# Kernel optimization log

Measured on AMD Instinct MI355X. Metric: run time of the kernel, lower is better.

Reference implementation:

```python
import jax, jax.numpy as jnp
import numpy as np

N, E = 100000, 800000
D_IN, D_H, D_EMB = 64, 64, 64
L, S = 2, 4
NOISE_SCALE, MIN_U = 0.1, 1e-6


def _xavier(k, shape):
    lim = float(np.sqrt(6.0 / (shape[0] + shape[1])))
    return jax.random.uniform(k, shape, jnp.float32, -lim, lim)


def setup_inputs():
    key = jax.random.key(0)
    ks = jax.random.split(key, 7)
    x = jax.random.normal(ks[0], (N, D_IN), jnp.float32)
    edge_index = jax.random.randint(ks[1], (2, E), 0, N)
    parent_mask = jax.random.bernoulli(ks[2], 0.7, (E,))
    Wi = _xavier(ks[3], (D_IN, D_H))
    bi = jnp.zeros((D_H,), jnp.float32)
    msg_W = jnp.stack([_xavier(jax.random.fold_in(ks[4], l), (2 * D_H, D_H)) for l in range(L)])
    msg_b = jnp.zeros((L, D_H), jnp.float32)
    upd_W = jnp.stack([_xavier(jax.random.fold_in(ks[5], l), (2 * D_H, D_H)) for l in range(L)])
    upd_b = jnp.zeros((L, D_H), jnp.float32)
    Wf = _xavier(ks[6], (D_H, D_EMB))
    bf = jnp.zeros((D_EMB,), jnp.float32)
    return dict(x=x, edge_index=edge_index, parent_mask=parent_mask, Wi=Wi, bi=bi,
                msg_W=msg_W, msg_b=msg_b, upd_W=upd_W, upd_b=upd_b, Wf=Wf, bf=bf)


def _gnn(x, src, dst, mask_f, cnt_inv, Wi, bi, msg_W, msg_b, upd_W, upd_b, Wf, bf):
    # input_proj -> relu, then L rounds of (gather -> message linear -> masked
    # scatter-mean -> update linear -> relu), then final_proj.
    h = jax.nn.relu(x @ Wi + bi)
    for l in range(L):
        Wm, Wu = msg_W[l], upd_W[l]
        # message = Linear(concat(x_i, x_j)); x_i = h[dst] (target), x_j = h[src] (source)
        msg = h[dst] @ Wm[:D_H] + h[src] @ Wm[D_H:] + msg_b[l]  # [E, D_H]
        agg = jax.ops.segment_sum(msg * mask_f[:, None], dst, num_segments=N) * cnt_inv[:, None]
        # update = Linear(concat(x, aggr_out))
        h = jax.nn.relu(h @ Wu[:D_H] + agg @ Wu[D_H:] + upd_b[l])
    return h @ Wf + bf  # [N, D_EMB]


def reference(x, edge_index, parent_mask, Wi, bi, msg_W, msg_b, upd_W, upd_b, Wf, bf):
    src, dst = edge_index[0], edge_index[1]
    mask_f = parent_mask.astype(x.dtype)
    # scatter-mean over causal-parent edges only (0 for nodes without parents, as in PyG)
    cnt = jax.ops.segment_sum(mask_f, dst, num_segments=N)
    cnt_inv = 1.0 / jnp.maximum(cnt, 1.0)
    params = (Wi, bi, msg_W, msg_b, upd_W, upd_b, Wf, bf)
    causal_z = _gnn(x, src, dst, mask_f, cnt_inv, *params)
    # Monte Carlo uncertainty: S perturbed causal embeddings, trace of sample covariance
    noise = jax.random.normal(jax.random.key(42), (S, N, D_IN), x.dtype) * NOISE_SCALE
    zs = jax.lax.map(lambda n: _gnn(x + n, src, dst, mask_f, cnt_inv, *params), noise)  # [S, N, D_EMB]
    mean = zs.mean(axis=0)
    u = jnp.sum((zs - mean[None]) ** 2, axis=(0, 2)) / (S - 1)
    u = jnp.maximum(u, MIN_U)
    return causal_z, u
```

## Files before the change

kernel.cpp:

```cpp
#include <hip/hip_runtime.h>
#include <stdint.h>

#define NN 100000
#define EE 800000
#define GEMM_BX 1563
#define WSTR 72
#define SLAB ((size_t)NN * 64)
#define EDGE_CAP 2304

typedef unsigned short u16;
typedef __attribute__((ext_vector_type(8))) short bf16x8;
typedef __attribute__((ext_vector_type(4))) float f32x4;

__device__ __forceinline__ uint32_t f2bf(float f) {
  uint32_t u = __float_as_uint(f);
  return (u + 0x7fffu + ((u >> 16) & 1u)) >> 16;
}

__device__ __forceinline__ void tf_round(uint32_t& x0, uint32_t& x1, int r) {
  x0 += x1;
  x1 = (x1 << r) | (x1 >> (32 - r));
  x1 ^= x0;
}

__device__ __forceinline__ void threefry_0_42(uint32_t c0, uint32_t c1,
                                              uint32_t& o0, uint32_t& o1) {
  const uint32_t ks0 = 0u, ks1 = 42u, ks2 = 0x1BD11BDAu ^ 42u;
  uint32_t x0 = c0 + ks0, x1 = c1 + ks1;
  tf_round(x0, x1, 13); tf_round(x0, x1, 15); tf_round(x0, x1, 26); tf_round(x0, x1, 6);
  x0 += ks1; x1 += ks2 + 1u;
  tf_round(x0, x1, 17); tf_round(x0, x1, 29); tf_round(x0, x1, 16); tf_round(x0, x1, 24);
  x0 += ks2; x1 += ks0 + 2u;
  tf_round(x0, x1, 13); tf_round(x0, x1, 15); tf_round(x0, x1, 26); tf_round(x0, x1, 6);
  x0 += ks0; x1 += ks1 + 3u;
  tf_round(x0, x1, 17); tf_round(x0, x1, 29); tf_round(x0, x1, 16); tf_round(x0, x1, 24);
  x0 += ks1; x1 += ks2 + 4u;
  tf_round(x0, x1, 13); tf_round(x0, x1, 15); tf_round(x0, x1, 26); tf_round(x0, x1, 6);
  x0 += ks2; x1 += ks0 + 5u;
  o0 = x0; o1 = x1;
}

__device__ __forceinline__ float noise_val(int s, int n, int d) {
  uint32_t f = (uint32_t)s * 6400000u + (uint32_t)n * 64u + (uint32_t)d;
  uint32_t o0, o1;
  threefry_0_42(0u, f, o0, o1);
  uint32_t bits = o0 ^ o1;
  float v = __uint_as_float((bits >> 9) | 0x3f800000u) - 1.0f;
  const float LO = -0.99999994f;
  float u = v * 2.0f + LO;
  u = fmaxf(u, LO);
  float w = -__logf(fmaf(-u, u, 1.0f));
  float ww = w - 2.5f;
  float p = 2.81022636e-08f;
  p = fmaf(p, ww, 3.43273939e-07f);
  p = fmaf(p, ww, -3.5233877e-06f);
  p = fmaf(p, ww, -4.39150654e-06f);
  p = fmaf(p, ww, 0.00021858087f);
  p = fmaf(p, ww, -0.00125372503f);
  p = fmaf(p, ww, -0.00417768164f);
  p = fmaf(p, ww, 0.246640727f);
  p = fmaf(p, ww, 1.50140941f);
  if (__any(w >= 5.0f)) {
    float ws = sqrtf(w) - 3.0f;
    float p2 = -0.000200214257f;
    p2 = fmaf(p2, ws, 0.000100950558f);
    p2 = fmaf(p2, ws, 0.00134934322f);
    p2 = fmaf(p2, ws, -0.00367342844f);
    p2 = fmaf(p2, ws, 0.00573950773f);
    p2 = fmaf(p2, ws, -0.0076224613f);
    p2 = fmaf(p2, ws, 0.00943887047f);
    p2 = fmaf(p2, ws, 1.00167406f);
    p2 = fmaf(p2, ws, 2.83297682f);
    p = (w < 5.0f) ? p : p2;
  }
  return 0.141421356f * (p * u);
}

__device__ __forceinline__ int mask_at(const void* m, int e, int mode) {
  if (mode == 0) return ((const int*)m)[e] != 0;
  if (mode == 1) return ((const unsigned char*)m)[e] != 0;
  return ((const float*)m)[e] != 0.0f;
}

__global__ void k_detect(const unsigned* mw, int* mode_out) {
  __shared__ int nonbin, nonfloat;
  if (threadIdx.x == 0) { nonbin = 0; nonfloat = 0; }
  __syncthreads();
  int lb = 0, lf = 0;
  for (int i = threadIdx.x; i < 4096; i += 256) {
    unsigned v = mw[i];
    if (v > 1u) lb = 1;
    if (v != 0u && v != 0x3F800000u) lf = 1;
  }
  if (lb) atomicOr(&nonbin, 1);
  if (lf) atomicOr(&nonfloat, 1);
  __syncthreads();
  if (threadIdx.x == 0)
    mode_out[0] = (nonbin == 0) ? 0 : ((nonfloat == 0) ? 2 : 1);
}

__global__ void k_count(const void* mask, const int* dst, int* cnt, const int* mode_p) {
  int e = blockIdx.x * 256 + threadIdx.x;
  if (e >= EE) return;
  if (mask_at(mask, e, *mode_p)) atomicAdd(&cnt[dst[e]], 1);
}

__global__ void k_scan_a(const int* cnt, int* blockSums) {
  __shared__ int sd[256];
  int t = threadIdx.x;
  int base = blockIdx.x * 1024 + t * 4;
  int s = 0;
  #pragma unroll
  for (int j = 0; j < 4; ++j) {
    int i = base + j;
    if (i < NN) s += cnt[i];
  }
  sd[t] = s;
  __syncthreads();
  for (int off = 128; off > 0; off >>= 1) {
    if (t < off) sd[t] += sd[t + off];
    __syncthreads();
  }
  if (t == 0) blockSums[blockIdx.x] = sd[0];
}

__global__ void k_scan_b(int* blockSums, int nb, int* total_out) {
  __shared__ int sd[128];
  int t = threadIdx.x;
  int v = (t < nb) ? blockSums[t] : 0;
  sd[t] = v;
  __syncthreads();
  for (int off = 1; off < 128; off <<= 1) {
    int x = (t >= off) ? sd[t - off] : 0;
    __syncthreads();
    sd[t] += x;
    __syncthreads();
  }
  if (t < nb) blockSums[t] = sd[t] - v;
  if (t == 0) total_out[0] = sd[127];
}

__global__ void k_scan_c(const int* cnt, const int* blockOffs, int* row_ptr,
                         int* cursor, float* cinv) {
  __shared__ int sd[256];
  int t = threadIdx.x;
  int base = blockIdx.x * 1024 + t * 4;
  int v[4], s = 0;
  #pragma unroll
  for (int j = 0; j < 4; ++j) {
    int i = base + j;
    v[j] = (i < NN) ? cnt[i] : 0;
    s += v[j];
  }
  sd[t] = s;
  __syncthreads();
  for (int off = 1; off < 256; off <<= 1) {
    int x = (t >= off) ? sd[t - off] : 0;
    __syncthreads();
    sd[t] += x;
    __syncthreads();
  }
  int excl = sd[t] - s + blockOffs[blockIdx.x];
  #pragma unroll
  for (int j = 0; j < 4; ++j) {
    int i = base + j;
    if (i < NN) {
      row_ptr[i] = excl;
      cursor[i] = excl;
      cinv[i] = 1.0f / fmaxf((float)v[j], 1.0f);
    }
    excl += v[j];
  }
}

__global__ void k_fill(const void* mask, const int* src, const int* dst,
                       int* cursor, int* col, const int* mode_p) {
  int e = blockIdx.x * 256 + threadIdx.x;
  if (e >= EE) return;
  if (mask_at(mask, e, *mode_p)) {
    int p = atomicAdd(&cursor[dst[e]], 1);
    col[p] = src[e];
  }
}

__global__ void k_prep(const float* msg_W, const float* msg_b, const float* upd_W,
                       const float* Wi, const float* Wf,
                       u16* Wu1T, u16* A1T, u16* A2T, float* C1,
                       u16* WiT, u16* WfT) {
  int t = threadIdx.x;
  int blk = blockIdx.x;
  if (blk >= 128) {
    const float* W = (blk == 128) ? Wi : Wf;
    u16* WT = (blk == 128) ? WiT : WfT;
    for (int o = t; o < 4096; o += 256) {
      int k = o >> 6, n = o & 63;
      WT[n * 64 + k] = (u16)f2bf(W[k * 64 + n]);
    }
    int l = blk - 128;
    const float* Wu2 = upd_W + l * 8192 + 4096;
    if (t < 64) {
      float acc = 0.f;
      for (int j = 0; j < 64; ++j) acc = fmaf(msg_b[l * 64 + j], Wu2[j * 64 + t], acc);
      C1[l * 64 + t] = acc;
    }
    return;
  }
  int l = blk >> 6, b = blk & 63;
  const float* WmT = msg_W + l * 8192;
  const float* WmB = WmT + 4096;
  const float* Wu1 = upd_W + l * 8192;
  const float* Wu2 = Wu1 + 4096;
  __shared__ float sd1[256], sd2[256];
  int a = t & 63, part = t >> 6;
  float a1 = 0.f, a2 = 0.f;
  #pragma unroll
  for (int jj = 0; jj < 16; ++jj) {
    int j = part * 16 + jj;
    float w2 = Wu2[j * 64 + b];
    a1 = fmaf(WmT[a * 64 + j], w2, a1);
    a2 = fmaf(WmB[a * 64 + j], w2, a2);
  }
  sd1[part * 64 + a] = a1;
  sd2[part * 64 + a] = a2;
  __syncthreads();
  if (t < 64) {
    float s1 = sd1[t] + sd1[64 + t] + sd1[128 + t] + sd1[192 + t];
    float s2 = sd2[t] + sd2[64 + t] + sd2[128 + t] + sd2[192 + t];
    int o = l * 4096 + b * 64 + t;
    A1T[o] = (u16)f2bf(s1);
    A2T[o] = (u16)f2bf(s2);
    Wu1T[o] = (u16)f2bf(Wu1[t * 64 + b]);
  }
}

__device__ __forceinline__ void mm4(const u16* lW, int m16, int q,
                                    bf16x8 a0, bf16x8 a1, f32x4 (&acc)[4]) {
  #pragma unroll
  for (int nt = 0; nt < 4; ++nt) {
    const u16* wp = lW + (nt * 16 + m16) * WSTR + q * 8;
    bf16x8 b0 = *(const bf16x8*)(wp);
    bf16x8 b1 = *(const bf16x8*)(wp + 32);
    acc[nt] = __builtin_amdgcn_mfma_f32_16x16x32_bf16(a0, b0, acc[nt], 0, 0, 0);
    acc[nt] = __builtin_amdgcn_mfma_f32_16x16x32_bf16(a1, b1, acc[nt], 0, 0, 0);
  }
}

__device__ __forceinline__ void stage_W(const u16* __restrict__ WT, u16* lW) {
  int t = threadIdx.x;
  int r = t >> 2, seg = (t & 3) * 16;
  const uint4* p = (const uint4*)(WT + r * 64 + seg);
  uint4 a = p[0], b = p[1];
  *(uint4*)(lW + r * WSTR + seg) = a;
  *(uint4*)(lW + r * WSTR + seg + 8) = b;
}

__device__ __forceinline__ void stage_H(const u16* __restrict__ Hin, int R0, u16* lT) {
  int t = threadIdx.x;
  int r = t >> 2, seg = (t & 3) * 16;
  int gr = R0 + r;
  uint4 a = {0, 0, 0, 0}, b = {0, 0, 0, 0};
  if (gr < NN) {
    const uint4* p = (const uint4*)(Hin + (size_t)gr * 64 + seg);
    a = p[0]; b = p[1];
  }
  *(uint4*)(lT + r * WSTR + seg) = a;
  *(uint4*)(lT + r * WSTR + seg + 8) = b;
}

__global__ __launch_bounds__(256) void k_input(const float* __restrict__ x,
                                               const u16* __restrict__ WiT,
                                               const float* __restrict__ bi,
                                               u16* __restrict__ HoutB) {
  __shared__ __align__(16) u16 lT[64 * WSTR];
  __shared__ __align__(16) u16 lW[64 * WSTR];
  __shared__ float lB[64];
  int t = threadIdx.x;
  int R0 = blockIdx.x * 64;
  int inst = blockIdx.y;
  u16* Hout = HoutB + (size_t)inst * SLAB;
  {
    int r = t >> 2, seg = (t & 3) * 16;
    int gr = R0 + r;
    float v[16];
    if (gr < NN) {
      const float4* xp = (const float4*)(x + (size_t)gr * 64 + seg);
      #pragma unroll
      for (int qq = 0; qq < 4; ++qq) {
        float4 f = xp[qq];
        v[qq * 4 + 0] = f.x; v[qq * 4 + 1] = f.y;
        v[qq * 4 + 2] = f.z; v[qq * 4 + 3] = f.w;
      }
      if (inst > 0) {
        int s = inst - 1;
        #pragma unroll
        for (int j = 0; j < 16; ++j) v[j] += noise_val(s, gr, seg + j);
      }
    } else {
      #pragma unroll
      for (int j = 0; j < 16; ++j) v[j] = 0.f;
    }
    uint32_t pk[8];
    #pragma unroll
    for (int j = 0; j < 8; ++j)
      pk[j] = f2bf(v[2 * j]) | (f2bf(v[2 * j + 1]) << 16);
    uint4 A = {pk[0], pk[1], pk[2], pk[3]};
    uint4 B = {pk[4], pk[5], pk[6], pk[7]};
    *(uint4*)(lT + r * WSTR + seg) = A;
    *(uint4*)(lT + r * WSTR + seg + 8) = B;
  }
  stage_W(WiT, lW);
  if (t < 64) lB[t] = bi[t];
  __syncthreads();
  int l = t & 63, w = t >> 6;
  int m16 = l & 15, q = l >> 4;
  const u16* aRow = lT + (w * 16 + m16) * WSTR + q * 8;
  bf16x8 fa0 = *(const bf16x8*)(aRow);
  bf16x8 fa1 = *(const bf16x8*)(aRow + 32);
  f32x4 acc[4] = {{0.f, 0.f, 0.f, 0.f}, {0.f, 0.f, 0.f, 0.f},
                  {0.f, 0.f, 0.f, 0.f}, {0.f, 0.f, 0.f, 0.f}};
  mm4(lW, m16, q, fa0, fa1, acc);
  #pragma unroll
  for (int nt = 0; nt < 4; ++nt) {
    int c = nt * 16 + m16;
    #pragma unroll
    for (int r_ = 0; r_ < 4; ++r_) {
      int row = w * 16 + q * 4 + r_;
      int gr = R0 + row;
      if (gr < NN) {
        float vv = fmaxf(acc[nt][r_] + lB[c], 0.f);
        Hout[(size_t)gr * 64 + c] = (u16)f2bf(vv);
      }
    }
  }
}

__global__ __launch_bounds__(256) void k_layer(const u16* __restrict__ HinB,
                                               u16* __restrict__ HoutB,
                                               const int* __restrict__ row_ptr,
                                               const int* __restrict__ col,
                                               const float* __restrict__ cinv,
                                               const u16* __restrict__ Wu1T,
                                               const u16* __restrict__ A1T,
                                               const u16* __restrict__ A2T,
                                               const float* __restrict__ b0,
                                               const float* __restrict__ c1) {
  __shared__ __align__(16) u16 lS0[64 * WSTR];
  __shared__ __align__(16) u16 lS1[64 * WSTR];
  __shared__ __align__(16) u16 lW[64 * WSTR];
  __shared__ float lB[128];
  __shared__ float lG[64];
  __shared__ int   lRP[65];
  int* lEdge = (int*)lW;

  int t = threadIdx.x;
  int R0 = blockIdx.x * 64;
  int instBase = blockIdx.y * 2;
  bool two = (instBase + 1) < 5;
  const u16* Hin0 = HinB + (size_t)instBase * SLAB;
  const u16* Hin1 = Hin0 + (two ? SLAB : 0);
  u16* Hout0 = HoutB + (size_t)instBase * SLAB;
  u16* Hout1 = Hout0 + SLAB;

  if (t < 65) {
    int idx = R0 + t;
    if (idx > NN) idx = NN;
    lRP[t] = row_ptr[idx];
  }
  if (t < 64) {
    lB[t] = b0[t];
    lB[64 + t] = c1[t];
  }
  __syncthreads();

  int e0 = lRP[0];
  int nE = lRP[64] - e0;
  bool inLds = (nE <= EDGE_CAP);
  if (inLds) {
    for (int i = t; i < nE; i += 256) lEdge[i] = col[e0 + i];
  }
  if (t < 64) lG[t] = (lRP[t + 1] > lRP[t]) ? 1.f : 0.f;
  __syncthreads();

  {
    int sub = t >> 3, lane8 = t & 7;
    int f0 = lane8 * 8;
    const u16* hb0 = Hin0 + f0;
    const u16* hb1 = Hin1 + f0;
    #pragma unroll
    for (int bb = 0; bb < 2; ++bb) {
      int r = bb * 32 + sub;
      int n = R0 + r;
      float g[8], h[8];
      #pragma unroll
      for (int j = 0; j < 8; ++j) { g[j] = 0.f; h[j] = 0.f; }
      if (n < NN) {
        int e = lRP[r], end = lRP[r + 1];
        int last = end - 1;
        for (; e < end; e += 4) {
          int idx4[4];
          #pragma unroll
          for (int j = 0; j < 4; ++j) {
            int ee = e + j;
            ee = (ee < last) ? ee : last;
            idx4[j] = inLds ? lEdge[ee - e0] : col[ee];
          }
          uint4 P[4];
          #pragma unroll
          for (int j = 0; j < 4; ++j)
            P[j] = *(const uint4*)(hb0 + ((unsigned)idx4[j] << 6));
          uint4 Q[4];
          if (two) {
            #pragma unroll
            for (int j = 0; j < 4; ++j)
              Q[j] = *(const uint4*)(hb1 + ((unsigned)idx4[j] << 6));
          }
          #pragma unroll
          for (int j = 1; j < 4; ++j) {
            bool ok = (e + j) < end;
            P[j].x = ok ? P[j].x : 0u;
            P[j].y = ok ? P[j].y : 0u;
            P[j].z = ok ? P[j].z : 0u;
            P[j].w = ok ? P[j].w : 0u;
            if (two) {
              Q[j].x = ok ? Q[j].x : 0u;
              Q[j].y = ok ? Q[j].y : 0u;
              Q[j].z = ok ? Q[j].z : 0u;
              Q[j].w = ok ? Q[j].w : 0u;
            }
          }
          #pragma unroll
          for (int j = 0; j < 4; ++j) {
            uint4 v = P[j];
            g[0] += __uint_as_float(v.x << 16);
            g[1] += __uint_as_float(v.x & 0xffff0000u);
            g[2] += __uint_as_float(v.y << 16);
            g[3] += __uint_as_float(v.y & 0xffff0000u);
            g[4] += __uint_as_float(v.z << 16);
            g[5] += __uint_as_float(v.z & 0xffff0000u);
            g[6] += __uint_as_float(v.w << 16);
            g[7] += __uint_as_float(v.w & 0xffff0000u);
          }
          if (two) {
            #pragma unroll
            for (int j = 0; j < 4; ++j) {
              uint4 v = Q[j];
              h[0] += __uint_as_float(v.x << 16);
              h[1] += __uint_as_float(v.x & 0xffff0000u);
              h[2] += __uint_as_float(v.y << 16);
              h[3] += __uint_as_float(v.y & 0xffff0000u);
              h[4] += __uint_as_float(v.z << 16);
              h[5] += __uint_as_float(v.z & 0xffff0000u);
              h[6] += __uint_as_float(v.w << 16);
              h[7] += __uint_as_float(v.w & 0xffff0000u);
            }
          }
        }
        float ci = cinv[n];
        #pragma unroll
        for (int j = 0; j < 8; ++j) { g[j] *= ci; h[j] *= ci; }
      }
      uint4 pk;
      pk.x = f2bf(g[0]) | (f2bf(g[1]) << 16);
      pk.y = f2bf(g[2]) | (f2bf(g[3]) << 16);
      pk.z = f2bf(g[4]) | (f2bf(g[5]) << 16);
      pk.w = f2bf(g[6]) | (f2bf(g[7]) << 16);
      *(uint4*)(lS0 + r * WSTR + f0) = pk;
      if (two) {
        uint4 pk2;
        pk2.x = f2bf(h[0]) | (f2bf(h[1]) << 16);
        pk2.y = f2bf(h[2]) | (f2bf(h[3]) << 16);
        pk2.z = f2bf(h[4]) | (f2bf(h[5]) << 16);
        pk2.w = f2bf(h[6]) | (f2bf(h[7]) << 16);
        *(uint4*)(lS1 + r * WSTR + f0) = pk2;
      }
    }
  }
  __syncthreads();

  int l = t & 63, w = t >> 6;
  int m16 = l & 15, q = l >> 4;
  int arow = w * 16 + m16;
  int gra = R0 + arow;
  bf16x8 zz = {0, 0, 0, 0, 0, 0, 0, 0};
  bf16x8 fa0_0 = zz, fa1_0 = zz, fa0_1 = zz, fa1_1 = zz;
  if (gra < NN) {
    const u16* ap = Hin0 + (size_t)gra * 64 + q * 8;
    fa0_0 = *(const bf16x8*)(ap);
    fa1_0 = *(const bf16x8*)(ap + 32);
    if (two) {
      const u16* ap1 = Hin1 + (size_t)gra * 64 + q * 8;
      fa0_1 = *(const bf16x8*)(ap1);
      fa1_1 = *(const bf16x8*)(ap1 + 32);
    }
  }

  stage_W(Wu1T, lW);
  __syncthreads();

  float gA = lG[arow];
  f32x4 acc0[4] = {{0.f, 0.f, 0.f, 0.f}, {0.f, 0.f, 0.f, 0.f},
                   {0.f, 0.f, 0.f, 0.f}, {0.f, 0.f, 0.f, 0.f}};
  f32x4 acc1[4] = {{0.f, 0.f, 0.f, 0.f}, {0.f, 0.f, 0.f, 0.f},
                   {0.f, 0.f, 0.f, 0.f}, {0.f, 0.f, 0.f, 0.f}};
  mm4(lW, m16, q, fa0_0, fa1_0, acc0);
  if (two) mm4(lW, m16, q, fa0_1, fa1_1, acc1);
  __syncthreads();
  stage_W(A1T, lW);
  __syncthreads();
  {
    bf16x8 ga0 = (gA != 0.f) ? fa0_0 : zz;
    bf16x8 ga1 = (gA != 0.f) ? fa1_0 : zz;
    mm4(lW, m16, q, ga0, ga1, acc0);
    if (two) {
      bf16x8 gb0 = (gA != 0.f) ? fa0_1 : zz;
      bf16x8 gb1 = (gA != 0.f) ? fa1_1 : zz;
      mm4(lW, m16, q, gb0, gb1, acc1);
    }
  }
  __syncthreads();
  stage_W(A2T, lW);
  __syncthreads();
  {
    const u16* sRow = lS0 + arow * WSTR + q * 8;
    bf16x8 fs0 = *(const bf16x8*)(sRow);
    bf16x8 fs1 = *(const bf16x8*)(sRow + 32);
    mm4(lW, m16, q, fs0, fs1, acc0);
    if (two) {
      const u16* sRow1 = lS1 + arow * WSTR + q * 8;
      bf16x8 ft0 = *(const bf16x8*)(sRow1);
      bf16x8 ft1 = *(const bf16x8*)(sRow1 + 32);
      mm4(lW, m16, q, ft0, ft1, acc1);
    }
  }
  #pragma unroll
  for (int nt = 0; nt < 4; ++nt) {
    int c = nt * 16 + m16;
    #pragma unroll
    for (int r_ = 0; r_ < 4; ++r_) {
      int row = w * 16 + q * 4 + r_;
      int gr = R0 + row;
      if (gr < NN) {
        float bias = lB[c] + lG[row] * lB[64 + c];
        float v0 = fmaxf(acc0[nt][r_] + bias, 0.f);
        Hout0[(size_t)gr * 64 + c] = (u16)f2bf(v0);
        if (two) {
          float v1 = fmaxf(acc1[nt][r_] + bias, 0.f);
          Hout1[(size_t)gr * 64 + c] = (u16)f2bf(v1);
        }
      }
    }
  }
}

__global__ __launch_bounds__(256) void k_final(const u16* __restrict__ HinB,
                                               const u16* __restrict__ WfT,
                                               const float* __restrict__ bfv,
                                               float* __restrict__ outCausal,
                                               float* __restrict__ out_u) {
  __shared__ __align__(16) u16 lT[64 * WSTR];
  __shared__ __align__(16) u16 lW[64 * WSTR];
  __shared__ float lB[64];
  int t = threadIdx.x;
  int R0 = blockIdx.x * 64;
  stage_W(WfT, lW);
  if (t < 64) lB[t] = bfv[t];
  int l = t & 63, w = t >> 6;
  int m16 = l & 15, q = l >> 4;
  float s1[16], s2[16];
  #pragma unroll
  for (int j = 0; j < 16; ++j) { s1[j] = 0.f; s2[j] = 0.f; }

  for (int inst = 0; inst < 5; ++inst) {
    __syncthreads();
    stage_H(HinB + (size_t)inst * SLAB, R0, lT);
    __syncthreads();
    const u16* aRow = lT + (w * 16 + m16) * WSTR + q * 8;
    bf16x8 fa0 = *(const bf16x8*)(aRow);
    bf16x8 fa1 = *(const bf16x8*)(aRow + 32);
    f32x4 acc[4] = {{0.f, 0.f, 0.f, 0.f}, {0.f, 0.f, 0.f, 0.f},
                    {0.f, 0.f, 0.f, 0.f}, {0.f, 0.f, 0.f, 0.f}};
    mm4(lW, m16, q, fa0, fa1, acc);
    #pragma unroll
    for (int nt = 0; nt < 4; ++nt) {
      int c = nt * 16 + m16;
      #pragma unroll
      for (int r_ = 0; r_ < 4; ++r_) {
        float z = acc[nt][r_] + lB[c];
        if (inst == 0) {
          int gr = R0 + w * 16 + q * 4 + r_;
          if (gr < NN) outCausal[(size_t)gr * 64 + c] = z;
        } else {
          s1[nt * 4 + r_] += z;
          s2[nt * 4 + r_] = fmaf(z, z, s2[nt * 4 + r_]);
        }
      }
    }
  }
  #pragma unroll
  for (int r_ = 0; r_ < 4; ++r_) {
    float pr = 0.f;
    #pragma unroll
    for (int nt = 0; nt < 4; ++nt) {
      float a = s1[nt * 4 + r_];
      pr += s2[nt * 4 + r_] - 0.25f * a * a;
    }
    #pragma unroll
    for (int msk = 1; msk < 16; msk <<= 1)
      pr += __shfl_xor(pr, msk, 64);
    if (m16 == 0) {
      int gr = R0 + w * 16 + q * 4 + r_;
      if (gr < NN) out_u[gr] = fmaxf(pr * (1.0f / 3.0f), 1e-6f);
    }
  }
}

extern "C" void kernel_launch(void* const* d_in, const int* in_sizes, int n_in,
                              void* d_out, int out_size, void* d_ws, size_t ws_size,
                              hipStream_t stream) {
  const float* x      = (const float*)d_in[0];
  const int*   eidx   = (const int*)d_in[1];
  const void*  mask   = d_in[2];
  const float* Wi     = (const float*)d_in[3];
  const float* bi     = (const float*)d_in[4];
  const float* msg_W  = (const float*)d_in[5];
  const float* msg_b  = (const float*)d_in[6];
  const float* upd_W  = (const float*)d_in[7];
  const float* upd_b  = (const float*)d_in[8];
  const float* Wf     = (const float*)d_in[9];
  const float* bfv    = (const float*)d_in[10];

  const int* src = eidx;
  const int* dst = eidx + EE;

  char* ws = (char*)d_ws;
  size_t off = 0;
  auto alloc = [&](size_t bytes) -> void* {
    void* p = ws + off;
    off += (bytes + 255) & ~(size_t)255;
    return p;
  };

  int*   cnt     = (int*)alloc(NN * sizeof(int));
  float* cinv    = (float*)alloc(NN * sizeof(float));
  int*   row_ptr = (int*)alloc((NN + 1) * sizeof(int));
  int*   cursor  = (int*)alloc(NN * sizeof(int));
  int*   col     = (int*)alloc(EE * sizeof(int));
  int*   bsums   = (int*)alloc(128 * sizeof(int));
  int*   mode_p  = (int*)alloc(sizeof(int));
  u16*   Wu1T    = (u16*)alloc(2 * 4096 * sizeof(u16));
  u16*   A1T     = (u16*)alloc(2 * 4096 * sizeof(u16));
  u16*   A2T     = (u16*)alloc(2 * 4096 * sizeof(u16));
  u16*   WiT     = (u16*)alloc(4096 * sizeof(u16));
  u16*   WfT     = (u16*)alloc(4096 * sizeof(u16));
  float* C1      = (float*)alloc(2 * 64 * sizeof(float));
  u16*   HA      = (u16*)alloc(5 * SLAB * sizeof(u16));
  u16*   HB      = (u16*)alloc(5 * SLAB * sizeof(u16));

  float* out_causal = (float*)d_out;
  float* out_u      = (float*)d_out + SLAB;

  k_detect<<<1, 256, 0, stream>>>((const unsigned*)mask, mode_p);
  hipMemsetAsync(cnt, 0, NN * sizeof(int), stream);
  k_count<<<EE / 256, 256, 0, stream>>>(mask, dst, cnt, mode_p);
  const int SCAN_BLKS = (NN + 1023) / 1024;
  k_scan_a<<<SCAN_BLKS, 256, 0, stream>>>(cnt, bsums);
  k_scan_b<<<1, 128, 0, stream>>>(bsums, SCAN_BLKS, row_ptr + NN);
  k_scan_c<<<SCAN_BLKS, 256, 0, stream>>>(cnt, bsums, row_ptr, cursor, cinv);
  k_fill<<<EE / 256, 256, 0, stream>>>(mask, src, dst, cursor, col, mode_p);

  k_prep<<<130, 256, 0, stream>>>(msg_W, msg_b, upd_W, Wi, Wf,
                                  Wu1T, A1T, A2T, C1, WiT, WfT);

  dim3 g5(GEMM_BX, 5);
  dim3 gl(GEMM_BX, 3);
  k_input<<<g5, 256, 0, stream>>>(x, WiT, bi, HA);
  k_layer<<<gl, 256, 0, stream>>>(HA, HB, row_ptr, col, cinv,
                                  Wu1T, A1T, A2T, upd_b, C1);
  k_layer<<<gl, 256, 0, stream>>>(HB, HA, row_ptr, col, cinv,
                                  Wu1T + 4096, A1T + 4096, A2T + 4096,
                                  upd_b + 64, C1 + 64);
  k_final<<<GEMM_BX, 256, 0, stream>>>(HA, WfT, bfv, out_causal, out_u);

  (void)in_sizes; (void)n_in; (void)out_size; (void)ws_size;
}
```

Baseline: 434.4 us.

## Fuse last GNN layer with final projection and variance; loop instances in input kernel

The second message-passing layer is merged with the final projection and uncertainty reduction, so each block runs all five instances in three passes and keeps the layer output in LDS. This avoids writing and re-reading the full hidden-state slabs between the last layer and the final kernel. The input projection kernel also loops over the five instances inside one block, loading x once instead of once per grid row. In exchange, parallelism drops from a 3-wide grid to one row of blocks, each doing sequential work, which may hurt latency hiding on the gather-heavy layer.

After: 471.9 us. +8.6%, slower.

```diff
diff --git a/kernel.cpp b/kernel.cpp
--- a/kernel.cpp
+++ b/kernel.cpp
@@ -254,19 +254,6 @@
   *(uint4*)(lW + r * WSTR + seg + 8) = b;
 }
 
-__device__ __forceinline__ void stage_H(const u16* __restrict__ Hin, int R0, u16* lT) {
-  int t = threadIdx.x;
-  int r = t >> 2, seg = (t & 3) * 16;
-  int gr = R0 + r;
-  uint4 a = {0, 0, 0, 0}, b = {0, 0, 0, 0};
-  if (gr < NN) {
-    const uint4* p = (const uint4*)(Hin + (size_t)gr * 64 + seg);
-    a = p[0]; b = p[1];
-  }
-  *(uint4*)(lT + r * WSTR + seg) = a;
-  *(uint4*)(lT + r * WSTR + seg + 8) = b;
-}
-
 __global__ __launch_bounds__(256) void k_input(const float* __restrict__ x,
                                                const u16* __restrict__ WiT,
                                                const float* __restrict__ bi,
@@ -276,61 +263,67 @@
   __shared__ float lB[64];
   int t = threadIdx.x;
   int R0 = blockIdx.x * 64;
-  int inst = blockIdx.y;
-  u16* Hout = HoutB + (size_t)inst * SLAB;
-  {
-    int r = t >> 2, seg = (t & 3) * 16;
-    int gr = R0 + r;
-    float v[16];
-    if (gr < NN) {
-      const float4* xp = (const float4*)(x + (size_t)gr * 64 + seg);
+  int r = t >> 2, seg = (t & 3) * 16;
+  int grs = R0 + r;
+  float v[16];
+  if (grs < NN) {
+    const float4* xp = (const float4*)(x + (size_t)grs * 64 + seg);
+    #pragma unroll
+    for (int qq = 0; qq < 4; ++qq) {
+      float4 f = xp[qq];
+      v[qq * 4 + 0] = f.x; v[qq * 4 + 1] = f.y;
+      v[qq * 4 + 2] = f.z; v[qq * 4 + 3] = f.w;
+    }
+  } else {
+    #pragma unroll
+    for (int j = 0; j < 16; ++j) v[j] = 0.f;
+  }
+  stage_W(WiT, lW);
+  if (t < 64) lB[t] = bi[t];
+
+  int l = t & 63, w = t >> 6;
+  int m16 = l & 15, q = l >> 4;
+
+  for (int inst = 0; inst < 5; ++inst) {
+    float vv[16];
+    #pragma unroll
+    for (int j = 0; j < 16; ++j) vv[j] = v[j];
+    if (inst > 0 && grs < NN) {
+      int s = inst - 1;
       #pragma unroll
-      for (int qq = 0; qq < 4; ++qq) {
-        float4 f = xp[qq];
-        v[qq * 4 + 0] = f.x; v[qq * 4 + 1] = f.y;
-        v[qq * 4 + 2] = f.z; v[qq * 4 + 3] = f.w;
-      }
-      if (inst > 0) {
-        int s = inst - 1;
-        #pragma unroll
-        for (int j = 0; j < 16; ++j) v[j] += noise_val(s, gr, seg + j);
-      }
-    } else {
-      #pragma unroll
-      for (int j = 0; j < 16; ++j) v[j] = 0.f;
+      for (int j = 0; j < 16; ++j) vv[j] += noise_val(s, grs, seg + j);
     }
     uint32_t pk[8];
     #pragma unroll
     for (int j = 0; j < 8; ++j)
-      pk[j] = f2bf(v[2 * j]) | (f2bf(v[2 * j + 1]) << 16);
+      pk[j] = f2bf(vv[2 * j]) | (f2bf(vv[2 * j + 1]) << 16);
     uint4 A = {pk[0], pk[1], pk[2], pk[3]};
     uint4 B = {pk[4], pk[5], pk[6], pk[7]};
     *(uint4*)(lT + r * WSTR + seg) = A;
     *(uint4*)(lT + r * WSTR + seg + 8) = B;
-  }
-  stage_W(WiT, lW);
-  if (t < 64) lB[t] = bi[t];
-  __syncthreads();
-  int l = t & 63, w = t >> 6;
-  int m16 = l & 15, q = l >> 4;
-  const u16* aRow = lT + (w * 16 + m16) * WSTR + q * 8;
-  bf16x8 fa0 = *(const bf16x8*)(aRow);
-  bf16x8 fa1 = *(const bf16x8*)(aRow + 32);
-  f32x4 acc[4] = {{0.f, 0.f, 0.f, 0.f}, {0.f, 0.f, 0.f, 0.f},
-                  {0.f, 0.f, 0.f, 0.f}, {0.f, 0.f, 0.f, 0.f}};
-  mm4(lW, m16, q, fa0, fa1, acc);
-  #pragma unroll
-  for (int nt = 0; nt < 4; ++nt) {
-    int c = nt * 16 + m16;
-    #pragma unroll
-    for (int r_ = 0; r_ < 4; ++r_) {
-      int row = w * 16 + q * 4 + r_;
-      int gr = R0 + row;
-      if (gr < NN) {
-        float vv = fmaxf(acc[nt][r_] + lB[c], 0.f);
-        Hout[(size_t)gr * 64 + c] = (u16)f2bf(vv);
-      }
-    }
+    __syncthreads();
+
+    const u16* aRow = lT + (w * 16 + m16) * WSTR + q * 8;
+    bf16x8 fa0 = *(const bf16x8*)(aRow);
+    bf16x8 fa1 = *(const bf16x8*)(aRow + 32);
+    f32x4 acc[4] = {{0.f, 0.f, 0.f, 0.f}, {0.f, 0.f, 0.f, 0.f},
+                    {0.f, 0.f, 0.f, 0.f}, {0.f, 0.f, 0.f, 0.f}};
+    mm4(lW, m16, q, fa0, fa1, acc);
+    u16* Hout = HoutB + (size_t)inst * SLAB;
+    #pragma unroll
+    for (int nt = 0; nt < 4; ++nt) {
+      int c = nt * 16 + m16;
+      #pragma unroll
+      for (int r_ = 0; r_ < 4; ++r_) {
+        int row = w * 16 + q * 4 + r_;
+        int gr = R0 + row;
+        if (gr < NN) {
+          float z = fmaxf(acc[nt][r_] + lB[c], 0.f);
+          Hout[(size_t)gr * 64 + c] = (u16)f2bf(z);
+        }
+      }
+    }
+    __syncthreads();
   }
 }
 
@@ -552,50 +545,273 @@
   }
 }
 
-__global__ __launch_bounds__(256) void k_final(const u16* __restrict__ HinB,
-                                               const u16* __restrict__ WfT,
-                                               const float* __restrict__ bfv,
-                                               float* __restrict__ outCausal,
-                                               float* __restrict__ out_u) {
-  __shared__ __align__(16) u16 lT[64 * WSTR];
+__global__ __launch_bounds__(256) void k_layer2f(const u16* __restrict__ HinB,
+                                                 const int* __restrict__ row_ptr,
+                                                 const int* __restrict__ col,
+                                                 const float* __restrict__ cinv,
+                                                 const u16* __restrict__ Wu1T,
+                                                 const u16* __restrict__ A1T,
+                                                 const u16* __restrict__ A2T,
+                                                 const u16* __restrict__ WfT,
+                                                 const float* __restrict__ b0,
+                                                 const float* __restrict__ c1,
+                                                 const float* __restrict__ bfv,
+                                                 float* __restrict__ outCausal,
+                                                 float* __restrict__ out_u) {
+  __shared__ __align__(16) u16 lS0[64 * WSTR];
+  __shared__ __align__(16) u16 lS1[64 * WSTR];
   __shared__ __align__(16) u16 lW[64 * WSTR];
-  __shared__ float lB[64];
+  __shared__ float lB[192];
+  __shared__ float lG[64];
+  __shared__ int   lRP[65];
+  int* lEdge = (int*)lW;
+
   int t = threadIdx.x;
   int R0 = blockIdx.x * 64;
-  stage_W(WfT, lW);
-  if (t < 64) lB[t] = bfv[t];
+  if (t < 65) {
+    int idx = R0 + t;
+    if (idx > NN) idx = NN;
+    lRP[t] = row_ptr[idx];
+  }
+  if (t < 64) {
+    lB[t] = b0[t];
+    lB[64 + t] = c1[t];
+    lB[128 + t] = bfv[t];
+  }
+  __syncthreads();
+  int e0 = lRP[0];
+  int nE = lRP[64] - e0;
+  bool inLds = (nE <= EDGE_CAP);
+  if (t < 64) lG[t] = (lRP[t + 1] > lRP[t]) ? 1.f : 0.f;
+
   int l = t & 63, w = t >> 6;
   int m16 = l & 15, q = l >> 4;
+  int arow = w * 16 + m16;
+  int gra = R0 + arow;
+  bf16x8 zz = {0, 0, 0, 0, 0, 0, 0, 0};
+
   float s1[16], s2[16];
   #pragma unroll
   for (int j = 0; j < 16; ++j) { s1[j] = 0.f; s2[j] = 0.f; }
 
-  for (int inst = 0; inst < 5; ++inst) {
-    __syncthreads();
-    stage_H(HinB + (size_t)inst * SLAB, R0, lT);
-    __syncthreads();
-    const u16* aRow = lT + (w * 16 + m16) * WSTR + q * 8;
-    bf16x8 fa0 = *(const bf16x8*)(aRow);
-    bf16x8 fa1 = *(const bf16x8*)(aRow + 32);
-    f32x4 acc[4] = {{0.f, 0.f, 0.f, 0.f}, {0.f, 0.f, 0.f, 0.f},
-                    {0.f, 0.f, 0.f, 0.f}, {0.f, 0.f, 0.f, 0.f}};
-    mm4(lW, m16, q, fa0, fa1, acc);
+  for (int p = 0; p < 3; ++p) {
+    int instBase = p * 2;
+    bool two = (instBase + 1) < 5;
+    const u16* Hin0 = HinB + (size_t)instBase * SLAB;
+    const u16* Hin1 = Hin0 + (two ? SLAB : 0);
+
+    __syncthreads();
+    if (inLds) {
+      for (int i = t; i < nE; i += 256) lEdge[i] = col[e0 + i];
+    }
+    __syncthreads();
+
+    {
+      int sub = t >> 3, lane8 = t & 7;
+      int f0 = lane8 * 8;
+      const u16* hb0 = Hin0 + f0;
+      const u16* hb1 = Hin1 + f0;
+      #pragma unroll
+      for (int bb = 0; bb < 2; ++bb) {
+        int r = bb * 32 + sub;
+        int n = R0 + r;
+        float g[8], h[8];
+        #pragma unroll
+        for (int j = 0; j < 8; ++j) { g[j] = 0.f; h[j] = 0.f; }
+        if (n < NN) {
+          int e = lRP[r], end = lRP[r + 1];
+          int last = end - 1;
+          for (; e < end; e += 4) {
+            int idx4[4];
+            #pragma unroll
+            for (int j = 0; j < 4; ++j) {
+              int ee = e + j;
+              ee = (ee < last) ? ee : last;
+              idx4[j] = inLds ? lEdge[ee - e0] : col[ee];
+            }
+            uint4 P[4];
+            #pragma unroll
+            for (int j = 0; j < 4; ++j)
+              P[j] = *(const uint4*)(hb0 + ((unsigned)idx4[j] << 6));
+            uint4 Q[4];
+            if (two) {
+              #pragma unroll
+              for (int j = 0; j < 4; ++j)
+                Q[j] = *(const uint4*)(hb1 + ((unsigned)idx4[j] << 6));
+            }
+            #pragma unroll
+            for (int j = 1; j < 4; ++j) {
+              bool ok = (e + j) < end;
+              P[j].x = ok ? P[j].x : 0u;
+              P[j].y = ok ? P[j].y : 0u;
+              P[j].z = ok ? P[j].z : 0u;
+              P[j].w = ok ? P[j].w : 0u;
+              if (two) {
+                Q[j].x = ok ? Q[j].x : 0u;
+                Q[j].y = ok ? Q[j].y : 0u;
+                Q[j].z = ok ? Q[j].z : 0u;
+                Q[j].w = ok ? Q[j].w : 0u;
+              }
+            }
+            #pragma unroll
+            for (int j = 0; j < 4; ++j) {
+              uint4 v = P[j];
+              g[0] += __uint_as_float(v.x << 16);
+              g[1] += __uint_as_float(v.x & 0xffff0000u);
+              g[2] += __uint_as_float(v.y << 16);
+              g[3] += __uint_as_float(v.y & 0xffff0000u);
+              g[4] += __uint_as_float(v.z << 16);
+              g[5] += __uint_as_float(v.z & 0xffff0000u);
+              g[6] += __uint_as_float(v.w << 16);
+              g[7] += __uint_as_float(v.w & 0xffff0000u);
+            }
+            if (two) {
+              #pragma unroll
+              for (int j = 0; j < 4; ++j) {
+                uint4 v = Q[j];
+                h[0] += __uint_as_float(v.x << 16);
+                h[1] += __uint_as_float(v.x & 0xffff0000u);
+                h[2] += __uint_as_float(v.y << 16);
+                h[3] += __uint_as_float(v.y & 0xffff0000u);
+                h[4] += __uint_as_float(v.z << 16);
+                h[5] += __uint_as_float(v.z & 0xffff0000u);
+                h[6] += __uint_as_float(v.w << 16);
+                h[7] += __uint_as_float(v.w & 0xffff0000u);
+              }
+            }
+          }
+          float ci = cinv[n];
+          #pragma unroll
+          for (int j = 0; j < 8; ++j) { g[j] *= ci; h[j] *= ci; }
+        }
+        uint4 pk;
+        pk.x = f2bf(g[0]) | (f2bf(g[1]) << 16);
+        pk.y = f2bf(g[2]) | (f2bf(g[3]) << 16);
+        pk.z = f2bf(g[4]) | (f2bf(g[5]) << 16);
+        pk.w = f2bf(g[6]) | (f2bf(g[7]) << 16);
+        *(uint4*)(lS0 + r * WSTR + f0) = pk;
+        if (two) {
+          uint4 pk2;
+          pk2.x = f2bf(h[0]) | (f2bf(h[1]) << 16);
+          pk2.y = f2bf(h[2]) | (f2bf(h[3]) << 16);
+          pk2.z = f2bf(h[4]) | (f2bf(h[5]) << 16);
+          pk2.w = f2bf(h[6]) | (f2bf(h[7]) << 16);
+          *(uint4*)(lS1 + r * WSTR + f0) = pk2;
+        }
+      }
+    }
+
+    bf16x8 fa0_0 = zz, fa1_0 = zz, fa0_1 = zz, fa1_1 = zz;
+    if (gra < NN) {
+      const u16* ap = Hin0 + (size_t)gra * 64 + q * 8;
+      fa0_0 = *(const bf16x8*)(ap);
+      fa1_0 = *(const bf16x8*)(ap + 32);
+      if (two) {
+        const u16* ap1 = Hin1 + (size_t)gra * 64 + q * 8;
+        fa0_1 = *(const bf16x8*)(ap1);
+        fa1_1 = *(const bf16x8*)(ap1 + 32);
+      }
+    }
+
+    __syncthreads();
+    stage_W(Wu1T, lW);
+    __syncthreads();
+
+    float gA = lG[arow];
+    f32x4 acc0[4] = {{0.f, 0.f, 0.f, 0.f}, {0.f, 0.f, 0.f, 0.f},
+                     {0.f, 0.f, 0.f, 0.f}, {0.f, 0.f, 0.f, 0.f}};
+    f32x4 acc1[4] = {{0.f, 0.f, 0.f, 0.f}, {0.f, 0.f, 0.f, 0.f},
+                     {0.f, 0.f, 0.f, 0.f}, {0.f, 0.f, 0.f, 0.f}};
+    mm4(lW, m16, q, fa0_0, fa1_0, acc0);
+    if (two) mm4(lW, m16, q, fa0_1, fa1_1, acc1);
+    __syncthreads();
+    stage_W(A1T, lW);
+    __syncthreads();
+    {
+      bf16x8 ga0 = (gA != 0.f) ? fa0_0 : zz;
+      bf16x8 ga1 = (gA != 0.f) ? fa1_0 : zz;
+      mm4(lW, m16, q, ga0, ga1, acc0);
+      if (two) {
+        bf16x8 gb0 = (gA != 0.f) ? fa0_1 : zz;
+        bf16x8 gb1 = (gA != 0.f) ? fa1_1 : zz;
+        mm4(lW, m16, q, gb0, gb1, acc1);
+      }
+    }
+    __syncthreads();
+    stage_W(A2T, lW);
+    __syncthreads();
+    {
+      const u16* sRow = lS0 + arow * WSTR + q * 8;
+      bf16x8 fs0 = *(const bf16x8*)(sRow);
+      bf16x8 fs1 = *(const bf16x8*)(sRow + 32);
+      mm4(lW, m16, q, fs0, fs1, acc0);
+      if (two) {
+        const u16* sRow1 = lS1 + arow * WSTR + q * 8;
+        bf16x8 ft0 = *(const bf16x8*)(sRow1);
+        bf16x8 ft1 = *(const bf16x8*)(sRow1 + 32);
+        mm4(lW, m16, q, ft0, ft1, acc1);
+      }
+    }
+
+    __syncthreads();
     #pragma unroll
     for (int nt = 0; nt < 4; ++nt) {
       int c = nt * 16 + m16;
       #pragma unroll
       for (int r_ = 0; r_ < 4; ++r_) {
-        float z = acc[nt][r_] + lB[c];
-        if (inst == 0) {
+        int row = w * 16 + q * 4 + r_;
+        float bias = lB[c] + lG[row] * lB[64 + c];
+        float v0 = fmaxf(acc0[nt][r_] + bias, 0.f);
+        lS0[row * WSTR + c] = (u16)f2bf(v0);
+        if (two) {
+          float v1 = fmaxf(acc1[nt][r_] + bias, 0.f);
+          lS1[row * WSTR + c] = (u16)f2bf(v1);
+        }
+      }
+    }
+    __syncthreads();
+    stage_W(WfT, lW);
+    __syncthreads();
+
+    f32x4 zac0[4] = {{0.f, 0.f, 0.f, 0.f}, {0.f, 0.f, 0.f, 0.f},
+                     {0.f, 0.f, 0.f, 0.f}, {0.f, 0.f, 0.f, 0.f}};
+    f32x4 zac1[4] = {{0.f, 0.f, 0.f, 0.f}, {0.f, 0.f, 0.f, 0.f},
+                     {0.f, 0.f, 0.f, 0.f}, {0.f, 0.f, 0.f, 0.f}};
+    {
+      const u16* hr0 = lS0 + arow * WSTR + q * 8;
+      bf16x8 hn00 = *(const bf16x8*)(hr0);
+      bf16x8 hn01 = *(const bf16x8*)(hr0 + 32);
+      mm4(lW, m16, q, hn00, hn01, zac0);
+      if (two) {
+        const u16* hr1 = lS1 + arow * WSTR + q * 8;
+        bf16x8 hn10 = *(const bf16x8*)(hr1);
+        bf16x8 hn11 = *(const bf16x8*)(hr1 + 32);
+        mm4(lW, m16, q, hn10, hn11, zac1);
+      }
+    }
+    #pragma unroll
+    for (int nt = 0; nt < 4; ++nt) {
+      int c = nt * 16 + m16;
+      #pragma unroll
+      for (int r_ = 0; r_ < 4; ++r_) {
+        int j = nt * 4 + r_;
+        float z0 = zac0[nt][r_] + lB[128 + c];
+        if (p == 0) {
           int gr = R0 + w * 16 + q * 4 + r_;
-          if (gr < NN) outCausal[(size_t)gr * 64 + c] = z;
+          if (gr < NN) outCausal[(size_t)gr * 64 + c] = z0;
         } else {
-          s1[nt * 4 + r_] += z;
-          s2[nt * 4 + r_] = fmaf(z, z, s2[nt * 4 + r_]);
+          s1[j] += z0;
+          s2[j] = fmaf(z0, z0, s2[j]);
         }
-      }
-    }
-  }
+        if (two) {
+          float z1 = zac1[nt][r_] + lB[128 + c];
+          s1[j] += z1;
+          s2[j] = fmaf(z1, z1, s2[j]);
+        }
+      }
+    }
+  }
+
   #pragma unroll
   for (int r_ = 0; r_ < 4; ++r_) {
     float pr = 0.f;
@@ -671,15 +887,14 @@
   k_prep<<<130, 256, 0, stream>>>(msg_W, msg_b, upd_W, Wi, Wf,
                                   Wu1T, A1T, A2T, C1, WiT, WfT);
 
-  dim3 g5(GEMM_BX, 5);
   dim3 gl(GEMM_BX, 3);
-  k_input<<<g5, 256, 0, stream>>>(x, WiT, bi, HA);
+  k_input<<<GEMM_BX, 256, 0, stream>>>(x, WiT, bi, HA);
   k_layer<<<gl, 256, 0, stream>>>(HA, HB, row_ptr, col, cinv,
                                   Wu1T, A1T, A2T, upd_b, C1);
-  k_layer<<<gl, 256, 0, stream>>>(HB, HA, row_ptr, col, cinv,
-                                  Wu1T + 4096, A1T + 4096, A2T + 4096,
-                                  upd_b + 64, C1 + 64);
-  k_final<<<GEMM_BX, 256, 0, stream>>>(HA, WfT, bfv, out_causal, out_u);
+  k_layer2f<<<GEMM_BX, 256, 0, stream>>>(HB, row_ptr, col, cinv,
+                                         Wu1T + 4096, A1T + 4096, A2T + 4096, WfT,
+                                         upd_b + 64, C1 + 64, bfv,
+                                         out_causal, out_u);
 
   (void)in_sizes; (void)n_in; (void)out_size; (void)ws_size;
 }
```

## Merge edge count, weight prep and input projection into one mega-kernel

Applied to the files above, without the earlier changes.

Fuses k_count, k_prep and k_input into a single k_mega launch whose block index selects the role: edge counting, Wf transpose with bias folding, message/update weight folding, or the input projection tiles. The input projection now converts and transposes Wi from fp32 in every block instead of reading a pre-staged bf16 transpose, which removes the dependency on the prep kernel. The goal is to save launch overhead and let independent work overlap on the GPU. In exchange, each of the 7815 input blocks redoes the Wi conversion with strided LDS writes.

Result: no change. 430.8 us (-0.8%).

```diff
diff --git a/kernel.cpp b/kernel.cpp
--- a/kernel.cpp
+++ b/kernel.cpp
@@ -7,6 +7,12 @@
 #define WSTR 72
 #define SLAB ((size_t)NN * 64)
 #define EDGE_CAP 2304
+
+#define MB_COUNT 3125
+#define MB_WFC   2
+#define MB_PREP  128
+#define MB_INPUT 7815
+#define MB_TOTAL (MB_COUNT + MB_WFC + MB_PREP + MB_INPUT)
 
 typedef unsigned short u16;
 typedef __attribute__((ext_vector_type(8))) short bf16x8;
@@ -99,12 +105,6 @@
     mode_out[0] = (nonbin == 0) ? 0 : ((nonfloat == 0) ? 2 : 1);
 }
 
-__global__ void k_count(const void* mask, const int* dst, int* cnt, const int* mode_p) {
-  int e = blockIdx.x * 256 + threadIdx.x;
-  if (e >= EE) return;
-  if (mask_at(mask, e, *mode_p)) atomicAdd(&cnt[dst[e]], 1);
-}
-
 __global__ void k_scan_a(const int* cnt, int* blockSums) {
   __shared__ int sd[256];
   int t = threadIdx.x;
@@ -183,56 +183,6 @@
   }
 }
 
-__global__ void k_prep(const float* msg_W, const float* msg_b, const float* upd_W,
-                       const float* Wi, const float* Wf,
-                       u16* Wu1T, u16* A1T, u16* A2T, float* C1,
-                       u16* WiT, u16* WfT) {
-  int t = threadIdx.x;
-  int blk = blockIdx.x;
-  if (blk >= 128) {
-    const float* W = (blk == 128) ? Wi : Wf;
-    u16* WT = (blk == 128) ? WiT : WfT;
-    for (int o = t; o < 4096; o += 256) {
-      int k = o >> 6, n = o & 63;
-      WT[n * 64 + k] = (u16)f2bf(W[k * 64 + n]);
-    }
-    int l = blk - 128;
-    const float* Wu2 = upd_W + l * 8192 + 4096;
-    if (t < 64) {
-      float acc = 0.f;
-      for (int j = 0; j < 64; ++j) acc = fmaf(msg_b[l * 64 + j], Wu2[j * 64 + t], acc);
-      C1[l * 64 + t] = acc;
-    }
-    return;
-  }
-  int l = blk >> 6, b = blk & 63;
-  const float* WmT = msg_W + l * 8192;
-  const float* WmB = WmT + 4096;
-  const float* Wu1 = upd_W + l * 8192;
-  const float* Wu2 = Wu1 + 4096;
-  __shared__ float sd1[256], sd2[256];
-  int a = t & 63, part = t >> 6;
-  float a1 = 0.f, a2 = 0.f;
-  #pragma unroll
-  for (int jj = 0; jj < 16; ++jj) {
-    int j = part * 16 + jj;
-    float w2 = Wu2[j * 64 + b];
-    a1 = fmaf(WmT[a * 64 + j], w2, a1);
-    a2 = fmaf(WmB[a * 64 + j], w2, a2);
-  }
-  sd1[part * 64 + a] = a1;
-  sd2[part * 64 + a] = a2;
-  __syncthreads();
-  if (t < 64) {
-    float s1 = sd1[t] + sd1[64 + t] + sd1[128 + t] + sd1[192 + t];
-    float s2 = sd2[t] + sd2[64 + t] + sd2[128 + t] + sd2[192 + t];
-    int o = l * 4096 + b * 64 + t;
-    A1T[o] = (u16)f2bf(s1);
-    A2T[o] = (u16)f2bf(s2);
-    Wu1T[o] = (u16)f2bf(Wu1[t * 64 + b]);
-  }
-}
-
 __device__ __forceinline__ void mm4(const u16* lW, int m16, int q,
                                     bf16x8 a0, bf16x8 a1, f32x4 (&acc)[4]) {
   #pragma unroll
@@ -267,17 +217,83 @@
   *(uint4*)(lT + r * WSTR + seg + 8) = b;
 }
 
-__global__ __launch_bounds__(256) void k_input(const float* __restrict__ x,
-                                               const u16* __restrict__ WiT,
-                                               const float* __restrict__ bi,
-                                               u16* __restrict__ HoutB) {
+__global__ __launch_bounds__(256) void k_mega(
+    const void* __restrict__ mask, const int* __restrict__ dst,
+    int* __restrict__ cnt, const int* __restrict__ mode_p,
+    const float* __restrict__ x, const float* __restrict__ Wi,
+    const float* __restrict__ bi, u16* __restrict__ HoutB,
+    const float* __restrict__ msg_W, const float* __restrict__ msg_b,
+    const float* __restrict__ upd_W, const float* __restrict__ Wf,
+    u16* __restrict__ Wu1T, u16* __restrict__ A1T, u16* __restrict__ A2T,
+    float* __restrict__ C1, u16* __restrict__ WfT) {
   __shared__ __align__(16) u16 lT[64 * WSTR];
   __shared__ __align__(16) u16 lW[64 * WSTR];
   __shared__ float lB[64];
   int t = threadIdx.x;
-  int R0 = blockIdx.x * 64;
-  int inst = blockIdx.y;
+  int bid = blockIdx.x;
+
+  if (bid < MB_COUNT) {
+    int e = bid * 256 + t;
+    if (e < EE && mask_at(mask, e, *mode_p)) atomicAdd(&cnt[dst[e]], 1);
+    return;
+  }
+  if (bid < MB_COUNT + MB_WFC) {
+    int l = bid - MB_COUNT;
+    if (l == 0) {
+      for (int o = t; o < 4096; o += 256) {
+        int k = o >> 6, n = o & 63;
+        WfT[n * 64 + k] = (u16)f2bf(Wf[k * 64 + n]);
+      }
+    }
+    const float* Wu2 = upd_W + l * 8192 + 4096;
+    if (t < 64) {
+      float acc = 0.f;
+      for (int j = 0; j < 64; ++j) acc = fmaf(msg_b[l * 64 + j], Wu2[j * 64 + t], acc);
+      C1[l * 64 + t] = acc;
+    }
+    return;
+  }
+  if (bid < MB_COUNT + MB_WFC + MB_PREP) {
+    int blk = bid - (MB_COUNT + MB_WFC);
+    int l = blk >> 6, b = blk & 63;
+    const float* WmT = msg_W + l * 8192;
+    const float* WmB = WmT + 4096;
+    const float* Wu1 = upd_W + l * 8192;
+    const float* Wu2 = Wu1 + 4096;
+    float* sd1 = (float*)lT;
+    float* sd2 = (float*)lW;
+    int a = t & 63, part = t >> 6;
+    float a1 = 0.f, a2 = 0.f;
+    #pragma unroll
+    for (int jj = 0; jj < 16; ++jj) {
+      int j = part * 16 + jj;
+      float w2 = Wu2[j * 64 + b];
+      a1 = fmaf(WmT[a * 64 + j], w2, a1);
+      a2 = fmaf(WmB[a * 64 + j], w2, a2);
+    }
+    sd1[part * 64 + a] = a1;
+    sd2[part * 64 + a] = a2;
+    __syncthreads();
+    if (t < 64) {
+      float s1 = sd1[t] + sd1[64 + t] + sd1[128 + t] + sd1[192 + t];
+      float s2 = sd2[t] + sd2[64 + t] + sd2[128 + t] + sd2[192 + t];
+      int o = l * 4096 + b * 64 + t;
+      A1T[o] = (u16)f2bf(s1);
+      A2T[o] = (u16)f2bf(s2);
+      Wu1T[o] = (u16)f2bf(Wu1[t * 64 + b]);
+    }
+    return;
+  }
+
+  int rel = bid - (MB_COUNT + MB_WFC + MB_PREP);
+  int tile = rel % GEMM_BX;
+  int inst = rel / GEMM_BX;
+  int R0 = tile * 64;
   u16* Hout = HoutB + (size_t)inst * SLAB;
+  for (int o = t; o < 4096; o += 256) {
+    int k = o >> 6, n = o & 63;
+    lW[n * WSTR + k] = (u16)f2bf(Wi[o]);
+  }
   {
     int r = t >> 2, seg = (t & 3) * 16;
     int gr = R0 + r;
@@ -308,7 +324,6 @@
     *(uint4*)(lT + r * WSTR + seg) = A;
     *(uint4*)(lT + r * WSTR + seg + 8) = B;
   }
-  stage_W(WiT, lW);
   if (t < 64) lB[t] = bi[t];
   __syncthreads();
   int l = t & 63, w = t >> 6;
@@ -650,7 +665,6 @@
   u16*   Wu1T    = (u16*)alloc(2 * 4096 * sizeof(u16));
   u16*   A1T     = (u16*)alloc(2 * 4096 * sizeof(u16));
   u16*   A2T     = (u16*)alloc(2 * 4096 * sizeof(u16));
-  u16*   WiT     = (u16*)alloc(4096 * sizeof(u16));
   u16*   WfT     = (u16*)alloc(4096 * sizeof(u16));
   float* C1      = (float*)alloc(2 * 64 * sizeof(float));
   u16*   HA      = (u16*)alloc(5 * SLAB * sizeof(u16));
@@ -661,19 +675,19 @@
 
   k_detect<<<1, 256, 0, stream>>>((const unsigned*)mask, mode_p);
   hipMemsetAsync(cnt, 0, NN * sizeof(int), stream);
-  k_count<<<EE / 256, 256, 0, stream>>>(mask, dst, cnt, mode_p);
+
+  k_mega<<<MB_TOTAL, 256, 0, stream>>>(mask, dst, cnt, mode_p,
+                                       x, Wi, bi, HA,
+                                       msg_W, msg_b, upd_W, Wf,
+                                       Wu1T, A1T, A2T, C1, WfT);
+
   const int SCAN_BLKS = (NN + 1023) / 1024;
   k_scan_a<<<SCAN_BLKS, 256, 0, stream>>>(cnt, bsums);
   k_scan_b<<<1, 128, 0, stream>>>(bsums, SCAN_BLKS, row_ptr + NN);
   k_scan_c<<<SCAN_BLKS, 256, 0, stream>>>(cnt, bsums, row_ptr, cursor, cinv);
   k_fill<<<EE / 256, 256, 0, stream>>>(mask, src, dst, cursor, col, mode_p);
 
-  k_prep<<<130, 256, 0, stream>>>(msg_W, msg_b, upd_W, Wi, Wf,
-                                  Wu1T, A1T, A2T, C1, WiT, WfT);
-
-  dim3 g5(GEMM_BX, 5);
   dim3 gl(GEMM_BX, 3);
-  k_input<<<g5, 256, 0, stream>>>(x, WiT, bi, HA);
   k_layer<<<gl, 256, 0, stream>>>(HA, HB, row_ptr, col, cinv,
                                   Wu1T, A1T, A2T, upd_b, C1);
   k_layer<<<gl, 256, 0, stream>>>(HB, HA, row_ptr, col, cinv,
```
